# Kernel optimization log

Measured on AMD Instinct MI355X. Metric: run time of the kernel, lower is better.

The kernel has to match this reference:

```python
import jax, jax.numpy as jnp
import numpy as np

B, S, C, T = 256, 128, 64, 60
ENC, COL, RNN, ATT, ACT, TYP = 512, 512, 512, 512, 128, 64
NPROD, NTYPE = 97, 32
LS, PTEMP, CTEMP = 0.2, 1.0, 1.0
NEG = -1e9


def setup_inputs() -> dict:
    key = jax.random.key(0)
    ks = jax.random.split(key, 24)
    enc = jax.random.normal(ks[0], (B, S, ENC), jnp.float32)
    col_enc = jax.random.normal(ks[1], (B, C, COL), jnp.float32)
    enc_lens = jax.random.randint(ks[2], (B,), 1, S + 1)
    col_lens = jax.random.randint(ks[3], (B,), 1, C + 1)
    action_kind = jax.random.randint(ks[4], (B, T), 0, 3)  # 0=ApplyRule,1=Reduce,2=SelectColumn
    tgt_lens = jax.random.randint(ks[5], (B,), 1, T + 1)
    prod_ids = jax.random.randint(ks[6], (B, T), 0, NPROD)
    col_ids = jax.random.randint(ks[7], (B, T), 0, C) % col_lens[:, None]
    parent_prod = jax.random.randint(ks[8], (B, T), 0, NPROD)
    parent_type = jax.random.randint(ks[9], (B, T), 0, NTYPE)
    parent_time = jax.random.randint(ks[10], (B, T), 0, T) % jnp.maximum(jnp.arange(T), 1)[None, :]
    g = lambda k, shp: jax.random.normal(k, shp, jnp.float32) * 0.02
    IN = ACT + ATT + ACT + TYP + RNN  # a_tm1 | att_tm1 | parent_prod | parent_type | parent_h
    return dict(
        enc=enc, col_enc=col_enc, enc_lens=enc_lens, col_lens=col_lens,
        action_kind=action_kind, tgt_lens=tgt_lens, prod_ids=prod_ids,
        col_ids=col_ids, parent_prod=parent_prod, parent_type=parent_type,
        parent_time=parent_time,
        prod_embed=g(ks[11], (NPROD + 1, ACT)),
        type_embed=g(ks[12], (NTYPE, TYP)),
        b_lin=jnp.zeros((NPROD + 1,), jnp.float32),
        W_ih=g(ks[13], (IN, 4 * RNN)), W_hh=g(ks[14], (RNN, 4 * RNN)),
        b_lstm=jnp.zeros((4 * RNN,), jnp.float32),
        W_att_q=g(ks[15], (RNN, ENC)),
        W_att_vec=g(ks[16], (ENC + RNN, ATT)),
        W_r1=g(ks[17], (ATT, 4 * ATT)), b_r1=jnp.zeros((4 * ATT,), jnp.float32),
        W_r2=g(ks[18], (4 * ATT, ACT)), b_r2=jnp.zeros((ACT,), jnp.float32),
        W_col_in=g(ks[19], (COL, ACT)),
        W_ptr=g(ks[20], (ATT, COL)),
        w_mem=g(ks[21], (ATT, 1)),
    )


def reference(enc, col_enc, enc_lens, col_lens, action_kind, tgt_lens, prod_ids,
              col_ids, parent_prod, parent_type, parent_time,
              prod_embed, type_embed, b_lin, W_ih, W_hh, b_lstm,
              W_att_q, W_att_vec, W_r1, b_r1, W_r2, b_r2,
              W_col_in, W_ptr, w_mem):
    enc_mask = jnp.arange(S)[None, :] < enc_lens[:, None]   # [B,S]
    col_valid = jnp.arange(C)[None, :] < col_lens[:, None]  # [B,C]
    col_in_embed = jnp.einsum('bcd,da->bca', col_enc, W_col_in)  # column_rnn_input, [B,C,ACT]

    # previous-step actions (a_{t-1}); dummy zeros at t=0 (x is zeroed there anyway)
    shift = lambda a: jnp.concatenate([jnp.zeros_like(a[:, :1]), a[:, :-1]], axis=1)
    kind_p, pid_p, cid_p = shift(action_kind), shift(prod_ids), shift(col_ids)

    def scan_step(carry, xs):
        h, c, att, hist, appear, acc = carry
        t, kp, pp, cp, kind, pid, cid, fprod, ftype, ptime = xs
        # --- prep step input ---
        prev_valid = (t - 1) < tgt_lens
        e_rule = prod_embed[jnp.where(kp == 1, NPROD, pp)]                      # [B,ACT]
        e_col = jnp.take_along_axis(col_in_embed, cp[:, None, None], axis=1)[:, 0]
        a_embed = jnp.where((kp == 2)[:, None], e_col, e_rule)
        a_embed = jnp.where(prev_valid[:, None], a_embed, 0.0)
        parent_h = hist[ptime, jnp.arange(B)]                                   # [B,RNN]
        x = jnp.concatenate([a_embed, att, prod_embed[fprod], type_embed[ftype], parent_h], axis=-1)
        x = jnp.where(t == 0, 0.0, x)
        # --- LSTMCell (torch gate order i,f,g,o) ---
        gates = x @ W_ih + h @ W_hh + b_lstm
        i, f, g_, o = jnp.split(gates, 4, axis=-1)
        c_new = jax.nn.sigmoid(f) * c + jax.nn.sigmoid(i) * jnp.tanh(g_)
        h_new = jax.nn.sigmoid(o) * jnp.tanh(c_new)
        # --- attention over encoder ---
        scores = jnp.einsum('bd,bsd->bs', h_new @ W_att_q, enc)
        scores = jnp.where(enc_mask, scores, NEG)
        ctx = jnp.einsum('bs,bsd->bd', jax.nn.softmax(scores, axis=-1), enc)
        att_new = jnp.tanh(jnp.concatenate([ctx, h_new], axis=-1) @ W_att_vec)
        # --- production readout (tied output embedding) ---
        emb_q = jnp.tanh(att_new @ W_r1 + b_r1) @ W_r2 + b_r2
        rule_lp = jax.nn.log_softmax((emb_q @ prod_embed.T + b_lin) / PTEMP, axis=-1)
        # --- pointer net over columns with memory gate ---
        gate = jax.nn.sigmoid(att_new @ w_mem)                                  # [B,1]
        w_c = jnp.einsum('bd,bcd->bc', att_new @ W_ptr, col_enc)
        weights = w_c * appear * gate + w_c * (1.0 - appear) * (1.0 - gate)
        weights = jnp.where(col_valid, weights, NEG) / CTEMP
        col_lp = jax.nn.log_softmax(weights, axis=-1)
        # --- per-example log prob of gold action ---
        valid = t < tgt_lens
        lp_rule = jnp.take_along_axis(rule_lp, jnp.where(kind == 1, NPROD, pid)[:, None], axis=1)[:, 0]
        lp_col_raw = jnp.take_along_axis(col_lp, cid[:, None], axis=1)[:, 0]
        col_sum = jnp.sum(jnp.where(col_valid, col_lp, 0.0), axis=-1)
        lp_col = (1.0 - LS) * lp_col_raw + LS * col_sum / col_lens
        lp = jnp.where(kind == 2, lp_col, lp_rule)
        acc = acc + jnp.where(valid, lp, 0.0)
        # --- state updates (appear mask updated after use, matching torch) ---
        appear = jnp.maximum(appear, ((kind == 2) & valid)[:, None] * jax.nn.one_hot(cid, C, dtype=appear.dtype))
        hist = hist.at[t].set(h_new)
        return (h_new, c_new, att_new, hist, appear, acc), None

    carry0 = (
        jnp.zeros((B, RNN), jnp.float32), jnp.zeros((B, RNN), jnp.float32),
        jnp.zeros((B, ATT), jnp.float32), jnp.zeros((T, B, RNN), jnp.float32),
        jnp.zeros((B, C), jnp.float32), jnp.zeros((B,), jnp.float32),
    )
    xs = (jnp.arange(T), kind_p.T, pid_p.T, cid_p.T, action_kind.T, prod_ids.T,
          col_ids.T, parent_prod.T, parent_type.T, parent_time.T)
    (_, _, _, _, _, acc), _ = jax.lax.scan(scan_step, carry0, xs)
    return -jnp.mean(acc)
```

## Files before the change

### kernel.cpp

```cpp
#include <hip/hip_runtime.h>
#include <math.h>

#define NB 256
#define NS 128
#define NCOL 64
#define NT 60
#define DENC 512
#define DRNN 512
#define DATT 512
#define DACT 128
#define DTYP 64
#define DG 2048
#define NEGV (-1e9f)
#define NBH 131072
#define NROW 15360
#define RPW 512
#define NRP 2624

typedef unsigned short ushort_t;
typedef __attribute__((ext_vector_type(8))) short short8;
typedef __attribute__((ext_vector_type(4))) float f32x4;

__device__ __forceinline__ float sigf(float x) { return 1.0f / (1.0f + __expf(-x)); }
__device__ __forceinline__ float tanhfast(float x) {
  x = fminf(fmaxf(x, -15.0f), 15.0f);
  float e = __expf(-2.0f * x);
  return (1.0f - e) / (1.0f + e);
}
__device__ __forceinline__ ushort_t f2bf(float f) {
  union { float f; unsigned u; } v; v.f = f;
  unsigned r = v.u + 0x7fffu + ((v.u >> 16) & 1u);
  return (ushort_t)(r >> 16);
}
__device__ __forceinline__ float bf2f(ushort_t b) {
  union { unsigned u; float f; } v; v.u = ((unsigned)b) << 16; return v.f;
}
__device__ __forceinline__ short8 cvt8(const float* p) {
  f32x4 x = *(const f32x4*)p, y = *(const f32x4*)(p + 4);
  short8 r;
  r[0]=(short)f2bf(x[0]); r[1]=(short)f2bf(x[1]); r[2]=(short)f2bf(x[2]); r[3]=(short)f2bf(x[3]);
  r[4]=(short)f2bf(y[0]); r[5]=(short)f2bf(y[1]); r[6]=(short)f2bf(y[2]); r[7]=(short)f2bf(y[3]);
  return r;
}

__global__ __launch_bounds__(256) void zero_kernel(float* __restrict__ p, int n) {
  int i = blockIdx.x * 256 + threadIdx.x;
  if (i < n) p[i] = 0.0f;
}

__global__ __launch_bounds__(256) void cvt_bf16_kernel(const float* __restrict__ src,
    ushort_t* __restrict__ dst, int n8)
{
  int i = blockIdx.x * 256 + threadIdx.x;
  if (i < n8) *(short8*)&dst[(size_t)i * 8] = cvt8(src + (size_t)i * 8);
}

__global__ __launch_bounds__(256) void pack_w(const float* __restrict__ src,
    ushort_t* __restrict__ dst, int Ksub, int Nsub, int Ntot, int K0, int N0, int ldsrc)
{
  int idx = blockIdx.x * 256 + threadIdx.x;
  if (idx >= Ksub * Nsub) return;
  int k = idx / Nsub, n = idx - k * Nsub;
  int gk = K0 + k;
  dst[((size_t)(gk >> 3) * Ntot + (N0 + n)) * 8 + (gk & 7)] =
      f2bf(src[(size_t)k * ldsrc + n]);
}

__global__ __launch_bounds__(256) void pack_wT(const float* __restrict__ W,
    ushort_t* __restrict__ dst)
{
  int idx = blockIdx.x * 256 + threadIdx.x;
  if (idx >= 512 * 512) return;
  int r = idx >> 9, d = idx & 511;
  dst[((size_t)(d >> 3) * 512 + r) * 8 + (d & 7)] = f2bf(W[(size_t)r * 512 + d]);
}

__global__ __launch_bounds__(256) void r2p_kernel(const float* __restrict__ W_r2,
    const float* __restrict__ prod_embed, const float* __restrict__ b_r2,
    const float* __restrict__ b_lin, ushort_t* __restrict__ Wr2p,
    float* __restrict__ bias2)
{
  int idx = blockIdx.x * 256 + threadIdx.x;
  if (idx >= 2049 * 98) return;
  int k = idx / 98, j = idx - k * 98;
  const float* pe = prod_embed + (size_t)j * DACT;
  if (k < 2048) {
    const float* wr = W_r2 + (size_t)k * DACT;
    float a = 0.f;
    #pragma unroll 8
    for (int d = 0; d < DACT; ++d) a = fmaf(wr[d], pe[d], a);
    Wr2p[((size_t)(k >> 3) * 128 + j) * 8 + (k & 7)] = f2bf(a);
  } else {
    float a = b_lin[j];
    #pragma unroll 8
    for (int d = 0; d < DACT; ++d) a = fmaf(b_r2[d], pe[d], a);
    bias2[j] = a;
  }
}

__global__ __launch_bounds__(64) void appear_kernel(const int* __restrict__ action_kind,
    const int* __restrict__ tgt_lens, const int* __restrict__ col_ids,
    float* __restrict__ appear_all)
{
  int b = blockIdx.x, c = threadIdx.x;
  float ap = 0.f;
  int tl = tgt_lens[b];
  for (int t = 0; t < NT; ++t) {
    appear_all[((size_t)t * NB + b) * 64 + c] = ap;
    if (t < tl && action_kind[b * NT + t] == 2 && col_ids[b * NT + t] == c) ap = 1.f;
  }
}

__global__ __launch_bounds__(256) void gemm_bf16(
    const float* __restrict__ A1, int lda1,
    const ushort_t* __restrict__ Bp, ushort_t* __restrict__ Cb, int ldc,
    int N, int K)
{
  __shared__ short As[2][4096];
  __shared__ short Bs[2][4096];
  const int tid = threadIdx.x;
  const int lane = tid & 63, w = tid >> 6;
  const int wr = w >> 1, wc = w & 1;
  const int mBase = blockIdx.y * 64, nBase = blockIdx.x * 64;
  const int nt = K >> 6;
  f32x4 ra0[2], ra1[2];
  short8 rb[2];
  auto issue = [&](int kt) {
    #pragma unroll
    for (int s = 0; s < 2; ++s) {
      int slot = tid + s * 256;
      int kc = slot >> 6, m = slot & 63;
      int k0 = (kt << 6) + kc * 8;
      const float* p = A1 + (size_t)(mBase + m) * lda1 + k0;
      ra0[s] = *(const f32x4*)p;
      ra1[s] = *(const f32x4*)(p + 4);
      rb[s] = *(const short8*)(Bp + ((size_t)(k0 >> 3) * N + nBase + m) * 8);
    }
  };
  auto store = [&](int buf) {
    #pragma unroll
    for (int s = 0; s < 2; ++s) {
      int slot = tid + s * 256;
      short8 av;
      av[0]=(short)f2bf(ra0[s][0]); av[1]=(short)f2bf(ra0[s][1]);
      av[2]=(short)f2bf(ra0[s][2]); av[3]=(short)f2bf(ra0[s][3]);
      av[4]=(short)f2bf(ra1[s][0]); av[5]=(short)f2bf(ra1[s][1]);
      av[6]=(short)f2bf(ra1[s][2]); av[7]=(short)f2bf(ra1[s][3]);
      *(short8*)&As[buf][slot * 8] = av;
      *(short8*)&Bs[buf][slot * 8] = rb[s];
    }
  };
  f32x4 z4 = {0.f,0.f,0.f,0.f};
  f32x4 acc[2][2] = {{z4,z4},{z4,z4}};
  issue(0); store(0);
  __syncthreads();
  int cur = 0;
  for (int kt = 0; kt < nt; ++kt) {
    bool more = (kt + 1 < nt);
    if (more) issue(kt + 1);
    #pragma unroll
    for (int kk = 0; kk < 2; ++kk) {
      int ko = kk * 4 + (lane >> 4);
      short8 af[2], bfr[2];
      #pragma unroll
      for (int f = 0; f < 2; ++f) {
        int row = wr * 32 + f * 16 + (lane & 15);
        af[f] = *(const short8*)&As[cur][(ko * 64 + row) * 8];
        int col = wc * 32 + f * 16 + (lane & 15);
        bfr[f] = *(const short8*)&Bs[cur][(ko * 64 + col) * 8];
      }
      #pragma unroll
      for (int i = 0; i < 2; ++i)
        #pragma unroll
        for (int j = 0; j < 2; ++j)
          acc[i][j] = __builtin_amdgcn_mfma_f32_16x16x32_bf16(af[i], bfr[j], acc[i][j], 0, 0, 0);
    }
    if (more) store(cur ^ 1);
    __syncthreads();
    cur ^= 1;
  }
  #pragma unroll
  for (int i = 0; i < 2; ++i)
    #pragma unroll
    for (int j = 0; j < 2; ++j)
      #pragma unroll
      for (int r = 0; r < 4; ++r) {
        int row = mBase + wr * 32 + i * 16 + (lane >> 4) * 4 + r;
        int col = nBase + wc * 32 + j * 16 + (lane & 15);
        Cb[(size_t)row * ldc + col] = f2bf(acc[i][j][r]);
      }
}

__global__ __launch_bounds__(256) void gemm_encwq(
    const float* __restrict__ enc, const ushort_t* __restrict__ WqTp,
    ushort_t* __restrict__ encWq, ushort_t* __restrict__ enc_b)
{
  __shared__ short Asm[32768];
  const int tid = threadIdx.x;
  const int lane = tid & 63, w = tid >> 6;
  const int wr = w >> 1, wc = w & 1;
  const int mBase = blockIdx.x * 64;
  #pragma unroll
  for (int it = 0; it < 16; ++it) {
    int o = tid + it * 256;
    int row = o >> 6, c = o & 63;
    short8 v = cvt8(enc + (size_t)(mBase + row) * 512 + c * 8);
    *(short8*)&Asm[row * 512 + ((c ^ (row & 7)) * 8)] = v;
    *(short8*)(enc_b + (size_t)(mBase + row) * 512 + c * 8) = v;
  }
  __syncthreads();
  for (int nt = 0; nt < 8; ++nt) {
    f32x4 z4 = {0.f,0.f,0.f,0.f};
    f32x4 acc[2][2] = {{z4,z4},{z4,z4}};
    short8 bb[2][4];
    auto loadBf = [&](int kt, short8* dst) {
      #pragma unroll
      for (int kk = 0; kk < 2; ++kk)
        #pragma unroll
        for (int f = 0; f < 2; ++f) {
          int ko = kt * 8 + kk * 4 + (lane >> 4);
          int col = nt * 64 + wc * 32 + f * 16 + (lane & 15);
          dst[kk * 2 + f] = *(const short8*)(WqTp + ((size_t)ko * 512 + col) * 8);
        }
    };
    loadBf(0, bb[0]);
    loadBf(1, bb[1]);
    #pragma unroll
    for (int kt = 0; kt < 8; ++kt) {
      short8 cur[4];
      #pragma unroll
      for (int i = 0; i < 4; ++i) cur[i] = bb[kt & 1][i];
      if (kt + 2 < 8) loadBf(kt + 2, bb[kt & 1]);
      #pragma unroll
      for (int kk = 0; kk < 2; ++kk) {
        int ko = kt * 8 + kk * 4 + (lane >> 4);
        short8 af[2];
        #pragma unroll
        for (int f = 0; f < 2; ++f) {
          int row = wr * 32 + f * 16 + (lane & 15);
          af[f] = *(const short8*)&Asm[row * 512 + ((ko ^ (row & 7)) * 8)];
        }
        #pragma unroll
        for (int i = 0; i < 2; ++i)
          #pragma unroll
          for (int j = 0; j < 2; ++j)
            acc[i][j] = __builtin_amdgcn_mfma_f32_16x16x32_bf16(af[i], cur[kk * 2 + j], acc[i][j], 0, 0, 0);
      }
    }
    #pragma unroll
    for (int i = 0; i < 2; ++i)
      #pragma unroll
      for (int j = 0; j < 2; ++j)
        #pragma unroll
        for (int r = 0; r < 4; ++r) {
          int row = mBase + wr * 32 + i * 16 + (lane >> 4) * 4 + r;
          int col = nt * 64 + wc * 32 + j * 16 + (lane & 15);
          encWq[(size_t)row * 512 + col] = f2bf(acc[i][j][r]);
        }
  }
}

template <class FA, class FB, class FE>
__device__ __forceinline__ void gemm_core(char* smem, FA loadA, FB loadB,
    int ktBeg, int ktEnd, FE epi)
{
  short* As = (short*)smem;
  short* Bs = (short*)smem + 8192;
  const int tid = threadIdx.x;
  const int lane = tid & 63, w = tid >> 6;
  const int wr = w >> 1, wc = w & 1;
  f32x4 z4 = {0.f,0.f,0.f,0.f};
  f32x4 acc[2][2] = {{z4,z4},{z4,z4}};
  short8 pa[2], pb[2];
  auto issue = [&](int kt) {
    #pragma unroll
    for (int s = 0; s < 2; ++s) {
      int slot = tid + s * 256;
      int kc = slot >> 6;
      int k = (kt << 6) + (kc << 3);
      pa[s] = loadA(k);
      pb[s] = loadB(slot & 63, k);
    }
  };
  auto store = [&](int buf) {
    #pragma unroll
    for (int s = 0; s < 2; ++s) {
      int slot = tid + s * 256;
      *(short8*)&As[buf * 4096 + slot * 8] = pa[s];
      *(short8*)&Bs[buf * 4096 + slot * 8] = pb[s];
    }
  };
  issue(ktBeg); store(0);
  __syncthreads();
  int cur = 0;
  for (int kt = ktBeg; kt < ktEnd; ++kt) {
    bool more = (kt + 1 < ktEnd);
    if (more) issue(kt + 1);
    #pragma unroll
    for (int kk = 0; kk < 2; ++kk) {
      int ko = kk * 4 + (lane >> 4);
      short8 af[2], bfr[2];
      #pragma unroll
      for (int f = 0; f < 2; ++f) {
        int row = wr * 32 + f * 16 + (lane & 15);
        af[f] = *(const short8*)&As[cur * 4096 + (ko * 64 + row) * 8];
        int col = wc * 32 + f * 16 + (lane & 15);
        bfr[f] = *(const short8*)&Bs[cur * 4096 + (ko * 64 + col) * 8];
      }
      #pragma unroll
      for (int i = 0; i < 2; ++i)
        #pragma unroll
        for (int j = 0; j < 2; ++j)
          acc[i][j] = __builtin_amdgcn_mfma_f32_16x16x32_bf16(af[i], bfr[j], acc[i][j], 0, 0, 0);
    }
    if (more) store(cur ^ 1);
    __syncthreads();
    cur ^= 1;
  }
  #pragma unroll
  for (int i = 0; i < 2; ++i)
    #pragma unroll
    for (int j = 0; j < 2; ++j)
      #pragma unroll
      for (int r = 0; r < 4; ++r) {
        int rl = wr * 32 + i * 16 + (lane >> 4) * 4 + r;
        int cl = wc * 32 + j * 16 + (lane & 15);
        epi(rl, cl, acc[i][j][r]);
      }
}

__global__ __launch_bounds__(256) void k1_gates(
    const int* __restrict__ action_kind, const int* __restrict__ tgt_lens,
    const int* __restrict__ prod_ids, const int* __restrict__ col_ids,
    const int* __restrict__ parent_prod, const int* __restrict__ parent_type,
    const int* __restrict__ parent_time,
    const float* __restrict__ prod_embed, const float* __restrict__ type_embed,
    const ushort_t* __restrict__ WpG, const ushort_t* __restrict__ colin_b,
    const ushort_t* __restrict__ att_all, const ushort_t* __restrict__ hist_u,
    float* __restrict__ gates0, float* __restrict__ gates1, int t)
{
  __shared__ __align__(16) char smem[32768];
  const int tid = threadIdx.x;
  const int nb = blockIdx.x, mb = blockIdx.y, ks = blockIdx.z;
  const int mBase = mb * 64, nBase = nb * 64;
  const int b = mBase + (tid & 63);
  int kp = action_kind[b * NT + t - 1];
  int pp = prod_ids[b * NT + t - 1];
  int cp = col_ids[b * NT + t - 1];
  bool pv = (t - 1) < tgt_lens[b];
  int fp = parent_prod[b * NT + t];
  int ft = parent_type[b * NT + t];
  int ptm = parent_time[b * NT + t];
  const ushort_t* hist_prev = hist_u + (size_t)(t - 1) * NBH;
  const ushort_t* att_prev = att_all + (size_t)(t - 1) * NB * DATT;
  auto loadA = [&](int k) -> short8 {
    short8 z = {0,0,0,0,0,0,0,0};
    if (k < 128) {
      if (!pv) return z;
      if (kp == 2) return *(const short8*)(colin_b + ((size_t)(b * NCOL + cp) * DACT + k));
      int row = (kp == 1) ? 97 : pp;
      return cvt8(prod_embed + (size_t)row * DACT + k);
    } else if (k < 640) {
      return *(const short8*)(att_prev + (size_t)b * DATT + (k - 128));
    } else if (k < 768) {
      return cvt8(prod_embed + (size_t)fp * DACT + (k - 640));
    } else if (k < 832) {
      return cvt8(type_embed + (size_t)ft * DTYP + (k - 768));
    } else if (k < 1344) {
      return *(const short8*)(hist_u + (size_t)ptm * NBH + (size_t)b * DRNN + (k - 832));
    } else {
      return *(const short8*)(hist_prev + (size_t)b * DRNN + (k - 1344));
    }
  };
  auto loadB = [&](int n, int k) -> short8 {
    return *(const short8*)(WpG + ((size_t)(k >> 3) * DG + nBase + n) * 8);
  };
  float* gp = ks ? gates1 : gates0;
  auto epi = [&](int rl, int cl, float v) {
    gp[(size_t)(mBase + rl) * DG + nBase + cl] = v;
  };
  gemm_core(smem, loadA, loadB, ks ? 15 : 0, ks ? 29 : 15, epi);
}

struct SmemK23 { float hq[DRNN]; float ml[4][2]; float cs[4][DENC]; };
__global__ __launch_bounds__(256) void k23_lstm_attn(
    const float* __restrict__ g0, const float* __restrict__ g1,
    const float* __restrict__ b_lstm, float* __restrict__ cst,
    ushort_t* __restrict__ hist_t,
    const ushort_t* __restrict__ encWq, const ushort_t* __restrict__ enc_b,
    const int* __restrict__ enc_lens, ushort_t* __restrict__ ctxb)
{
  __shared__ __align__(16) SmemK23 s;
  int b = blockIdx.x, tid = threadIdx.x;
  const float* p0 = g0 + (size_t)b * DG;
  const float* p1 = g1 + (size_t)b * DG;
  #pragma unroll
  for (int r = 0; r < 2; ++r) {
    int j = tid + r * 256;
    float gi = p0[j]        + p1[j]        + b_lstm[j];
    float gf = p0[512 + j]  + p1[512 + j]  + b_lstm[512 + j];
    float gg = p0[1024 + j] + p1[1024 + j] + b_lstm[1024 + j];
    float go = p0[1536 + j] + p1[1536 + j] + b_lstm[1536 + j];
    size_t ix = (size_t)b * DRNN + j;
    float cn = sigf(gf) * cst[ix] + sigf(gi) * tanhfast(gg);
    float hn = sigf(go) * tanhfast(cn);
    cst[ix] = cn;
    hist_t[ix] = f2bf(hn);
    s.hq[j] = hn;
  }
  __syncthreads();
  int w = tid >> 6, lane = tid & 63;
  int el = enc_lens[b];
  float q[8];
  #pragma unroll
  for (int j = 0; j < 8; ++j) q[j] = s.hq[lane * 8 + j];
  float m = -1e30f, lr = 0.f;
  float cacc[8];
  #pragma unroll
  for (int j = 0; j < 8; ++j) cacc[j] = 0.f;
  const ushort_t* eWb = encWq + (size_t)b * NS * DENC + lane * 8;
  const ushort_t* eb = enc_b + (size_t)b * NS * DENC + lane * 8;
  for (int sI = w; sI < el; sI += 4) {
    short8 xr = *(const short8*)(eWb + (size_t)sI * DENC);
    short8 er = *(const short8*)(eb + (size_t)sI * DENC);
    float d = 0.f;
    #pragma unroll
    for (int j = 0; j < 8; ++j) d = fmaf(bf2f((ushort_t)xr[j]), q[j], d);
    #pragma unroll
    for (int off = 32; off > 0; off >>= 1) d += __shfl_xor(d, off);
    float mn = fmaxf(m, d);
    float rr = __expf(m - mn), p = __expf(d - mn);
    lr = lr * rr + p;
    #pragma unroll
    for (int j = 0; j < 8; ++j) cacc[j] = cacc[j] * rr + p * bf2f((ushort_t)er[j]);
    m = mn;
  }
  if (lane == 0) { s.ml[w][0] = m; s.ml[w][1] = lr; }
  #pragma unroll
  for (int j = 0; j < 8; ++j) s.cs[w][lane * 8 + j] = cacc[j];
  __syncthreads();
  float M = fmaxf(fmaxf(s.ml[0][0], s.ml[1][0]), fmaxf(s.ml[2][0], s.ml[3][0]));
  float f0 = __expf(s.ml[0][0] - M), f1 = __expf(s.ml[1][0] - M);
  float f2 = __expf(s.ml[2][0] - M), f3 = __expf(s.ml[3][0] - M);
  float invL = 1.f / (f0 * s.ml[0][1] + f1 * s.ml[1][1] + f2 * s.ml[2][1] + f3 * s.ml[3][1]);
  #pragma unroll
  for (int rep = 0; rep < 2; ++rep) {
    int d = tid + rep * 256;
    ctxb[(size_t)b * DENC + d] =
        f2bf((f0 * s.cs[0][d] + f1 * s.cs[1][d] + f2 * s.cs[2][d] + f3 * s.cs[3][d]) * invL);
  }
}

__global__ __launch_bounds__(256) void k4_attvec(const ushort_t* __restrict__ ctxb,
    const ushort_t* __restrict__ hist_t, const ushort_t* __restrict__ WpV,
    ushort_t* __restrict__ att_all, int t)
{
  __shared__ __align__(16) char smem[32768];
  const int tid = threadIdx.x;
  const int mBase = blockIdx.y * 64, nBase = blockIdx.x * 64;
  const int b = mBase + (tid & 63);
  auto loadA = [&](int k) -> short8 {
    if (k < 512) return *(const short8*)(ctxb + (size_t)b * DENC + k);
    return *(const short8*)(hist_t + (size_t)b * DRNN + (k - 512));
  };
  auto loadB = [&](int n, int k) -> short8 {
    return *(const short8*)(WpV + ((size_t)(k >> 3) * 512 + nBase + n) * 8);
  };
  auto epi = [&](int rl, int cl, float v) {
    att_all[((size_t)t * NB + mBase + rl) * DATT + nBase + cl] = f2bf(tanhfast(v));
  };
  gemm_core(smem, loadA, loadB, 0, 16, epi);
}

__global__ __launch_bounds__(256) void kbig_r1ptr(const ushort_t* __restrict__ att_all,
    const ushort_t* __restrict__ WpRP, const float* __restrict__ b_r1,
    ushort_t* __restrict__ r1c, ushort_t* __restrict__ ptrq_all,
    float* __restrict__ gate_all, int rowBase)
{
  __shared__ __align__(16) char smem[32768];
  const int tid = threadIdx.x;
  const int mBase = blockIdx.y * 64, nBase = blockIdx.x * 64;
  const size_t grow = (size_t)rowBase + mBase + (tid & 63);
  auto loadA = [&](int k) -> short8 {
    return *(const short8*)(att_all + grow * DATT + k);
  };
  auto loadB = [&](int n, int k) -> short8 {
    return *(const short8*)(WpRP + ((size_t)(k >> 3) * NRP + nBase + n) * 8);
  };
  auto epi = [&](int rl, int cl, float v) {
    int col = nBase + cl;
    size_t gr = (size_t)rowBase + mBase + rl;
    if (col < 2048)      r1c[(size_t)(mBase + rl) * DG + col] = f2bf(tanhfast(v + b_r1[col]));
    else if (col < 2560) ptrq_all[gr * RPW + (col - 2048)] = f2bf(v);
    else if (col == 2560) gate_all[gr] = v;
  };
  gemm_core(smem, loadA, loadB, 0, 8, epi);
}

__global__ __launch_bounds__(256) void klogits(const ushort_t* __restrict__ r1c,
    const ushort_t* __restrict__ Wr2p, float* __restrict__ logits_all, int rowBase)
{
  __shared__ __align__(16) char smem[32768];
  const int tid = threadIdx.x;
  const int mBase = blockIdx.y * 64, nBase = blockIdx.x * 64;
  auto loadA = [&](int k) -> short8 {
    return *(const short8*)(r1c + (size_t)(mBase + (tid & 63)) * DG + k);
  };
  auto loadB = [&](int n, int k) -> short8 {
    return *(const short8*)(Wr2p + ((size_t)(k >> 3) * 128 + nBase + n) * 8);
  };
  auto epi = [&](int rl, int cl, float v) {
    logits_all[((size_t)rowBase + mBase + rl) * 128 + nBase + cl] = v;
  };
  gemm_core(smem, loadA, loadB, 0, 32, epi);
}

__global__ __launch_bounds__(256) void kwc(const ushort_t* __restrict__ ptrq_all,
    const ushort_t* __restrict__ colenc_b, float* __restrict__ w_c_all)
{
  __shared__ __align__(16) char smem[32768];
  const int tid = threadIdx.x;
  const int b = blockIdx.x;
  const int tt = tid & 63;
  auto loadA = [&](int k) -> short8 {
    short8 z = {0,0,0,0,0,0,0,0};
    if (tt >= NT) return z;
    return *(const short8*)(ptrq_all + ((size_t)tt * NB + b) * RPW + k);
  };
  auto loadB = [&](int n, int k) -> short8 {
    return *(const short8*)(colenc_b + ((size_t)b * NCOL + n) * 512 + k);
  };
  auto epi = [&](int rl, int cl, float v) {
    if (rl < NT) w_c_all[((size_t)rl * NB + b) * 64 + cl] = v;
  };
  gemm_core(smem, loadA, loadB, 0, 8, epi);
}

__global__ __launch_bounds__(64) void kfinal(
    const float* __restrict__ logits_all, const float* __restrict__ bias2,
    const float* __restrict__ w_c_all, const float* __restrict__ gate_all,
    const float* __restrict__ appear_all, const int* __restrict__ col_lens,
    const int* __restrict__ tgt_lens, const int* __restrict__ action_kind,
    const int* __restrict__ prod_ids, const int* __restrict__ col_ids,
    float* __restrict__ loss_tb)
{
  int row = blockIdx.x;
  int t = row >> 8, b = row & 255;
  int c = threadIdx.x;
  float l0 = logits_all[(size_t)row * 128 + c] + bias2[c];
  float l1 = (c + 64 < 98) ? logits_all[(size_t)row * 128 + 64 + c] + bias2[64 + c] : -1e30f;
  float m = fmaxf(l0, l1);
  #pragma unroll
  for (int off = 32; off > 0; off >>= 1) m = fmaxf(m, __shfl_down(m, off));
  m = __shfl(m, 0);
  float sv = __expf(l0 - m) + ((c + 64 < 98) ? __expf(l1 - m) : 0.f);
  #pragma unroll
  for (int off = 32; off > 0; off >>= 1) sv += __shfl_down(sv, off);
  sv = __shfl(sv, 0);
  float lseR = m + __logf(sv);
  int clen = col_lens[b];
  float gate = sigf(gate_all[row]);
  float ap = appear_all[(size_t)row * 64 + c];
  float wc = w_c_all[(size_t)row * 64 + c];
  float wv = wc * (ap * gate + (1.f - ap) * (1.f - gate));
  wv = (c < clen) ? wv : NEGV;
  float m2 = wv;
  #pragma unroll
  for (int off = 32; off > 0; off >>= 1) m2 = fmaxf(m2, __shfl_down(m2, off));
  m2 = __shfl(m2, 0);
  float s2 = __expf(wv - m2);
  #pragma unroll
  for (int off = 32; off > 0; off >>= 1) s2 += __shfl_down(s2, off);
  s2 = __shfl(s2, 0);
  float lse2 = m2 + __logf(s2);
  float csum = (c < clen) ? (wv - lse2) : 0.f;
  #pragma unroll
  for (int off = 32; off > 0; off >>= 1) csum += __shfl_down(csum, off);
  int kind = action_kind[b * NT + t];
  int cid = col_ids[b * NT + t];
  float wcid = __shfl(wv, cid);
  if (c == 0) {
    int pid = prod_ids[b * NT + t];
    bool valid = t < tgt_lens[b];
    int gj = (kind == 1) ? 97 : pid;
    float lgj = logits_all[(size_t)row * 128 + gj] + bias2[gj];
    float lp_rule = lgj - lseR;
    float lp_col = 0.8f * (wcid - lse2) + 0.2f * csum / (float)clen;
    float lp = (kind == 2) ? lp_col : lp_rule;
    loss_tb[row] = valid ? lp : 0.f;
  }
}

__global__ __launch_bounds__(256) void loss_reduce(const float* __restrict__ loss_tb,
                                                   float* __restrict__ out) {
  int tid = threadIdx.x;
  float v = 0.f;
  for (int k = 0; k < NT; ++k) v += loss_tb[(size_t)k * NB + tid];
  #pragma unroll
  for (int off = 32; off > 0; off >>= 1) v += __shfl_down(v, off);
  __shared__ float part[4];
  if ((tid & 63) == 0) part[tid >> 6] = v;
  __syncthreads();
  if (tid == 0) out[0] = -(part[0] + part[1] + part[2] + part[3]) * (1.0f / NB);
}

extern "C" void kernel_launch(void* const* d_in, const int* in_sizes, int n_in,
                              void* d_out, int out_size, void* d_ws, size_t ws_size,
                              hipStream_t stream) {
  const float* enc         = (const float*)d_in[0];
  const float* col_enc     = (const float*)d_in[1];
  const int*   enc_lens    = (const int*)d_in[2];
  const int*   col_lens    = (const int*)d_in[3];
  const int*   action_kind = (const int*)d_in[4];
  const int*   tgt_lens    = (const int*)d_in[5];
  const int*   prod_ids    = (const int*)d_in[6];
  const int*   col_ids     = (const int*)d_in[7];
  const int*   parent_prod = (const int*)d_in[8];
  const int*   parent_type = (const int*)d_in[9];
  const int*   parent_time = (const int*)d_in[10];
  const float* prod_embed  = (const float*)d_in[11];
  const float* type_embed  = (const float*)d_in[12];
  const float* b_lin       = (const float*)d_in[13];
  const float* W_ih        = (const float*)d_in[14];
  const float* W_hh        = (const float*)d_in[15];
  const float* b_lstm      = (const float*)d_in[16];
  const float* W_att_q     = (const float*)d_in[17];
  const float* W_att_vec   = (const float*)d_in[18];
  const float* W_r1        = (const float*)d_in[19];
  const float* b_r1        = (const float*)d_in[20];
  const float* W_r2        = (const float*)d_in[21];
  const float* b_r2        = (const float*)d_in[22];
  const float* W_col_in    = (const float*)d_in[23];
  const float* W_ptr       = (const float*)d_in[24];
  const float* w_mem       = (const float*)d_in[25];

  float* base = (float*)d_ws;
  size_t o = 0;
  float* cst    = base + o; o += 131072;
  float* gates0 = base + o; o += 524288;
  float* gates1 = base + o; o += 524288;
  int zeroN = (int)o;
  ushort_t* hist_u = (ushort_t*)(base + o); o += 3932160;
  float* logits_all = (float*)hist_u;
  ushort_t* colin_b = (ushort_t*)(base + o); o += 1048576;
  float* encWq_f    = base + o; o += 8388608;
  ushort_t* encWq   = (ushort_t*)encWq_f;
  ushort_t* r1c     = (ushort_t*)encWq_f;
  float* encb_f     = base + o; o += 4194304;
  ushort_t* enc_b   = (ushort_t*)encb_f;
  ushort_t* colenc_b = (ushort_t*)encb_f;
  ushort_t* att_all  = (ushort_t*)(base + o); o += 3932160;
  ushort_t* ptrq_all = (ushort_t*)(base + o); o += 3932160;
  ushort_t* ctxb     = ptrq_all;
  float* gate_all    = base + o; o += 15360;
  float* w_c_all     = base + o; o += 983040;
  float* appear_all  = base + o; o += 983040;
  float* loss_tb     = base + o; o += 15360;
  ushort_t* WpG   = (ushort_t*)(base + o); o += 1900544;
  ushort_t* WqTp  = (ushort_t*)(base + o); o += 131072;
  ushort_t* WpV   = (ushort_t*)(base + o); o += 262144;
  ushort_t* WpRP  = (ushort_t*)(base + o); o += 671744;
  ushort_t* WpCI  = (ushort_t*)(base + o); o += 32768;
  ushort_t* Wr2p  = (ushort_t*)(base + o); o += 131072;
  float* bias2    = base + o; o += 128;
  (void)ws_size; (void)in_sizes; (void)n_in; (void)out_size;

  zero_kernel<<<(zeroN + 255) / 256, 256, 0, stream>>>(base, zeroN);
  zero_kernel<<<(671744 + 255) / 256, 256, 0, stream>>>((float*)WpRP, 671744);
  zero_kernel<<<(131072 + 255) / 256, 256, 0, stream>>>((float*)Wr2p, 131072);

  pack_w<<<(1344 * 2048 + 255) / 256, 256, 0, stream>>>(W_ih, WpG, 1344, 2048, 2048, 0, 0, 2048);
  pack_w<<<(512 * 2048 + 255) / 256, 256, 0, stream>>>(W_hh, WpG, 512, 2048, 2048, 1344, 0, 2048);
  pack_wT<<<(512 * 512 + 255) / 256, 256, 0, stream>>>(W_att_q, WqTp);
  pack_w<<<(1024 * 512 + 255) / 256, 256, 0, stream>>>(W_att_vec, WpV, 1024, 512, 512, 0, 0, 512);
  pack_w<<<(512 * 2048 + 255) / 256, 256, 0, stream>>>(W_r1, WpRP, 512, 2048, NRP, 0, 0, 2048);
  pack_w<<<(512 * 512 + 255) / 256, 256, 0, stream>>>(W_ptr, WpRP, 512, 512, NRP, 0, 2048, 512);
  pack_w<<<(512 + 255) / 256, 256, 0, stream>>>(w_mem, WpRP, 512, 1, NRP, 0, 2560, 1);
  pack_w<<<(512 * 128 + 255) / 256, 256, 0, stream>>>(W_col_in, WpCI, 512, 128, 128, 0, 0, 128);
  r2p_kernel<<<(2049 * 98 + 255) / 256, 256, 0, stream>>>(W_r2, prod_embed, b_r2, b_lin, Wr2p, bias2);
  appear_kernel<<<NB, 64, 0, stream>>>(action_kind, tgt_lens, col_ids, appear_all);

  gemm_bf16<<<dim3(2, 256), 256, 0, stream>>>(col_enc, 512, WpCI, colin_b, 128, 128, 512);
  gemm_encwq<<<512, 256, 0, stream>>>(enc, WqTp, encWq, enc_b);

  for (int t = 0; t < NT; ++t) {
    ushort_t* hist_t = hist_u + (size_t)t * NBH;
    if (t > 0)
      k1_gates<<<dim3(32, 4, 2), 256, 0, stream>>>(
          action_kind, tgt_lens, prod_ids, col_ids, parent_prod, parent_type,
          parent_time, prod_embed, type_embed, WpG, colin_b, att_all, hist_u,
          gates0, gates1, t);
    k23_lstm_attn<<<NB, 256, 0, stream>>>(gates0, gates1, b_lstm, cst, hist_t,
                                          encWq, enc_b, enc_lens, ctxb);
    k4_attvec<<<dim3(8, 4), 256, 0, stream>>>(ctxb, hist_t, WpV, att_all, t);
  }

  cvt_bf16_kernel<<<(1048576 + 255) / 256, 256, 0, stream>>>(col_enc, colenc_b, 1048576);
  for (int ch = 0; ch < 2; ++ch) {
    int rowBase = ch * 7680;
    kbig_r1ptr<<<dim3(41, 120), 256, 0, stream>>>(att_all, WpRP, b_r1, r1c,
                                                  ptrq_all, gate_all, rowBase);
    klogits<<<dim3(2, 120), 256, 0, stream>>>(r1c, Wr2p, logits_all, rowBase);
  }
  kwc<<<NB, 256, 0, stream>>>(ptrq_all, colenc_b, w_c_all);
  kfinal<<<NROW, 64, 0, stream>>>(logits_all, bias2, w_c_all, gate_all,
      appear_all, col_lens, tgt_lens, action_kind, prod_ids, col_ids, loss_tb);
  loss_reduce<<<1, 256, 0, stream>>>(loss_tb, (float*)d_out);
}
```

Baseline: 3.390 ms.

## Split gates GEMM K four ways, remap blocks for XCD locality, transpose ptrq layout

The per-step gates GEMM now splits its K dimension across four blocks instead of two, doubling the block count so more CUs are busy during the latency-bound recurrent loop. The LSTM kernel sums four partial buffers instead of two, which adds memory traffic. The big r1/ptr and logits GEMMs use a 1D grid remapped so consecutive blocks on the same XCD (bid&7) share M-tiles for better L2 reuse. ptrq is stored batch-major so kwc reads contiguous rows.

```diff
diff --git a/kernel.cpp b/kernel.cpp
--- a/kernel.cpp
+++ b/kernel.cpp
@@ -337,7 +337,8 @@
     const float* __restrict__ prod_embed, const float* __restrict__ type_embed,
     const ushort_t* __restrict__ WpG, const ushort_t* __restrict__ colin_b,
     const ushort_t* __restrict__ att_all, const ushort_t* __restrict__ hist_u,
-    float* __restrict__ gates0, float* __restrict__ gates1, int t)
+    float* __restrict__ gates0, float* __restrict__ gates1,
+    float* __restrict__ gates2, float* __restrict__ gates3, int t)
 {
   __shared__ __align__(16) char smem[32768];
   const int tid = threadIdx.x;
@@ -375,16 +376,19 @@
   auto loadB = [&](int n, int k) -> short8 {
     return *(const short8*)(WpG + ((size_t)(k >> 3) * DG + nBase + n) * 8);
   };
-  float* gp = ks ? gates1 : gates0;
+  float* gp = (ks == 0) ? gates0 : (ks == 1) ? gates1 : (ks == 2) ? gates2 : gates3;
   auto epi = [&](int rl, int cl, float v) {
     gp[(size_t)(mBase + rl) * DG + nBase + cl] = v;
   };
-  gemm_core(smem, loadA, loadB, ks ? 15 : 0, ks ? 29 : 15, epi);
+  const int kb0 = (ks == 0) ? 0 : (ks == 1) ? 8 : (ks == 2) ? 15 : 22;
+  const int kb1 = (ks == 0) ? 8 : (ks == 1) ? 15 : (ks == 2) ? 22 : 29;
+  gemm_core(smem, loadA, loadB, kb0, kb1, epi);
 }
 
 struct SmemK23 { float hq[DRNN]; float ml[4][2]; float cs[4][DENC]; };
 __global__ __launch_bounds__(256) void k23_lstm_attn(
     const float* __restrict__ g0, const float* __restrict__ g1,
+    const float* __restrict__ g2, const float* __restrict__ g3,
     const float* __restrict__ b_lstm, float* __restrict__ cst,
     ushort_t* __restrict__ hist_t,
     const ushort_t* __restrict__ encWq, const ushort_t* __restrict__ enc_b,
@@ -394,13 +398,15 @@
   int b = blockIdx.x, tid = threadIdx.x;
   const float* p0 = g0 + (size_t)b * DG;
   const float* p1 = g1 + (size_t)b * DG;
+  const float* p2 = g2 + (size_t)b * DG;
+  const float* p3 = g3 + (size_t)b * DG;
   #pragma unroll
   for (int r = 0; r < 2; ++r) {
     int j = tid + r * 256;
-    float gi = p0[j]        + p1[j]        + b_lstm[j];
-    float gf = p0[512 + j]  + p1[512 + j]  + b_lstm[512 + j];
-    float gg = p0[1024 + j] + p1[1024 + j] + b_lstm[1024 + j];
-    float go = p0[1536 + j] + p1[1536 + j] + b_lstm[1536 + j];
+    float gi = p0[j] + p1[j] + p2[j] + p3[j] + b_lstm[j];
+    float gf = p0[512+j] + p1[512+j] + p2[512+j] + p3[512+j] + b_lstm[512+j];
+    float gg = p0[1024+j] + p1[1024+j] + p2[1024+j] + p3[1024+j] + b_lstm[1024+j];
+    float go = p0[1536+j] + p1[1536+j] + p2[1536+j] + p3[1536+j] + b_lstm[1536+j];
     size_t ix = (size_t)b * DRNN + j;
     float cn = sigf(gf) * cst[ix] + sigf(gi) * tanhfast(gg);
     float hn = sigf(go) * tanhfast(cn);
@@ -479,7 +485,11 @@
 {
   __shared__ __align__(16) char smem[32768];
   const int tid = threadIdx.x;
-  const int mBase = blockIdx.y * 64, nBase = blockIdx.x * 64;
+  const int bid = blockIdx.x;
+  const int x = bid & 7, j = bid >> 3;
+  const int mb = x * 15 + j / 41;
+  const int nb = j % 41;
+  const int mBase = mb * 64, nBase = nb * 64;
   const size_t grow = (size_t)rowBase + mBase + (tid & 63);
   auto loadA = [&](int k) -> short8 {
     return *(const short8*)(att_all + grow * DATT + k);
@@ -491,7 +501,7 @@
     int col = nBase + cl;
     size_t gr = (size_t)rowBase + mBase + rl;
     if (col < 2048)      r1c[(size_t)(mBase + rl) * DG + col] = f2bf(tanhfast(v + b_r1[col]));
-    else if (col < 2560) ptrq_all[gr * RPW + (col - 2048)] = f2bf(v);
+    else if (col < 2560) ptrq_all[((size_t)(gr & 255) * NT + (gr >> 8)) * RPW + (col - 2048)] = f2bf(v);
     else if (col == 2560) gate_all[gr] = v;
   };
   gemm_core(smem, loadA, loadB, 0, 8, epi);
@@ -502,7 +512,11 @@
 {
   __shared__ __align__(16) char smem[32768];
   const int tid = threadIdx.x;
-  const int mBase = blockIdx.y * 64, nBase = blockIdx.x * 64;
+  const int bid = blockIdx.x;
+  const int x = bid & 7, j = bid >> 3;
+  const int mb = x * 15 + (j >> 1);
+  const int nb = j & 1;
+  const int mBase = mb * 64, nBase = nb * 64;
   auto loadA = [&](int k) -> short8 {
     return *(const short8*)(r1c + (size_t)(mBase + (tid & 63)) * DG + k);
   };
@@ -525,7 +539,7 @@
   auto loadA = [&](int k) -> short8 {
     short8 z = {0,0,0,0,0,0,0,0};
     if (tt >= NT) return z;
-    return *(const short8*)(ptrq_all + ((size_t)tt * NB + b) * RPW + k);
+    return *(const short8*)(ptrq_all + ((size_t)b * NT + tt) * RPW + k);
   };
   auto loadB = [&](int n, int k) -> short8 {
     return *(const short8*)(colenc_b + ((size_t)b * NCOL + n) * 512 + k);
@@ -639,6 +653,8 @@
   float* cst    = base + o; o += 131072;
   float* gates0 = base + o; o += 524288;
   float* gates1 = base + o; o += 524288;
+  float* gates2 = base + o; o += 524288;
+  float* gates3 = base + o; o += 524288;
   int zeroN = (int)o;
   ushort_t* hist_u = (ushort_t*)(base + o); o += 3932160;
   float* logits_all = (float*)hist_u;
@@ -686,21 +702,21 @@
   for (int t = 0; t < NT; ++t) {
     ushort_t* hist_t = hist_u + (size_t)t * NBH;
     if (t > 0)
-      k1_gates<<<dim3(32, 4, 2), 256, 0, stream>>>(
+      k1_gates<<<dim3(32, 4, 4), 256, 0, stream>>>(
           action_kind, tgt_lens, prod_ids, col_ids, parent_prod, parent_type,
           parent_time, prod_embed, type_embed, WpG, colin_b, att_all, hist_u,
-          gates0, gates1, t);
-    k23_lstm_attn<<<NB, 256, 0, stream>>>(gates0, gates1, b_lstm, cst, hist_t,
-                                          encWq, enc_b, enc_lens, ctxb);
+          gates0, gates1, gates2, gates3, t);
+    k23_lstm_attn<<<NB, 256, 0, stream>>>(gates0, gates1, gates2, gates3,
+        b_lstm, cst, hist_t, encWq, enc_b, enc_lens, ctxb);
     k4_attvec<<<dim3(8, 4), 256, 0, stream>>>(ctxb, hist_t, WpV, att_all, t);
   }
 
   cvt_bf16_kernel<<<(1048576 + 255) / 256, 256, 0, stream>>>(col_enc, colenc_b, 1048576);
   for (int ch = 0; ch < 2; ++ch) {
     int rowBase = ch * 7680;
-    kbig_r1ptr<<<dim3(41, 120), 256, 0, stream>>>(att_all, WpRP, b_r1, r1c,
-                                                  ptrq_all, gate_all, rowBase);
-    klogits<<<dim3(2, 120), 256, 0, stream>>>(r1c, Wr2p, logits_all, rowBase);
+    kbig_r1ptr<<<4920, 256, 0, stream>>>(att_all, WpRP, b_r1, r1c,
+                                         ptrq_all, gate_all, rowBase);
+    klogits<<<240, 256, 0, stream>>>(r1c, Wr2p, logits_all, rowBase);
   }
   kwc<<<NB, 256, 0, stream>>>(ptrq_all, colenc_b, w_c_all);
   kfinal<<<NROW, 64, 0, stream>>>(logits_all, bias2, w_c_all, gate_all,
```

Result: faster. 3.072 ms (-9.4%).
